# Performance work log

Measured on AMD Instinct MI355X. Metric: run time of the kernel, lower is better.

Reference implementation:

```python
import jax, jax.numpy as jnp
from jax import lax
import numpy as np


def crf_log_likelihood(logits, tags, seqlen, trans):
    # logits [B,T,L], tags [B,T] int, seqlen [B] int, trans [L,L]
    B, T, L = logits.shape
    mask = jnp.arange(T)[None, :] < seqlen[:, None]  # [B,T] bool
    unary = jnp.take_along_axis(logits, tags[..., None], axis=2)[..., 0]  # [B,T]
    unary_score = jnp.sum(unary * mask, axis=1)
    binary = trans[tags[:, :-1], tags[:, 1:]]  # [B,T-1]
    binary_score = jnp.sum(binary * mask[:, 1:], axis=1)

    def step(alpha, inp):
        logit_t, m = inp  # [B,L], [B]
        new = jax.nn.logsumexp(alpha[:, :, None] + trans[None], axis=1) + logit_t
        return jnp.where(m[:, None], new, alpha), None

    xs = (jnp.moveaxis(logits[:, 1:], 1, 0), jnp.moveaxis(mask[:, 1:], 1, 0))
    alphaT, _ = lax.scan(step, logits[:, 0], xs)
    log_norm = jax.nn.logsumexp(alphaT, axis=1)  # [B]
    return unary_score + binary_score - log_norm


def crf_decode(logits, trans, seqlen):
    B, T, L = logits.shape
    mask = jnp.arange(T)[None, :] < seqlen[:, None]
    ident = jnp.broadcast_to(jnp.arange(L)[None, :], (B, L))

    def fwd(alpha, inp):
        logit_t, m = inp
        scores = alpha[:, :, None] + trans[None]  # [B,L,L]
        bp = jnp.argmax(scores, axis=1)  # [B,L] best prev tag for each cur tag
        new = jnp.max(scores, axis=1) + logit_t
        alpha = jnp.where(m[:, None], new, alpha)
        bp = jnp.where(m[:, None], bp, ident)  # identity bp on padded steps
        return alpha, bp

    xs = (jnp.moveaxis(logits[:, 1:], 1, 0), jnp.moveaxis(mask[:, 1:], 1, 0))
    alphaT, bps = lax.scan(fwd, logits[:, 0], xs)  # bps [T-1,B,L]
    last = jnp.argmax(alphaT, axis=1)  # [B]

    def back(tag, bp):
        prev = jnp.take_along_axis(bp, tag[:, None], axis=1)[:, 0]
        return prev, prev

    _, tags_prev = lax.scan(back, last, bps, reverse=True)  # [T-1,B]
    return jnp.concatenate([jnp.moveaxis(tags_prev, 1, 0), last[:, None]], axis=1)


def setup_inputs():
    key = jax.random.key(0)
    ks = jax.random.split(key, 8)
    B, T, D = 64, 512, 768
    L1, L2 = 2, 9
    x = jax.random.normal(ks[0], (B, T, D), dtype=jnp.float32)
    label = jax.random.randint(ks[1], (B, T), 0, L2)
    seqlen = jax.random.randint(ks[2], (B,), 1, T + 1)
    W1 = jax.random.truncated_normal(ks[3], -2.0, 2.0, (D, L1), jnp.float32) * 0.02
    b1 = jnp.zeros((L1,), jnp.float32)
    W2 = jax.random.truncated_normal(ks[4], -2.0, 2.0, (D, L2), jnp.float32) * 0.02
    b2 = jnp.zeros((L2,), jnp.float32)
    lim1 = float(np.sqrt(6.0 / (L1 + L1)))
    trans1 = jax.random.uniform(ks[5], (L1, L1), jnp.float32, -lim1, lim1)
    lim2 = float(np.sqrt(6.0 / (L2 + L2)))
    trans2 = jax.random.uniform(ks[6], (L2, L2), jnp.float32, -lim2, lim2)
    return {"x": x, "label": label, "seqlen": seqlen, "W1": W1, "b1": b1,
            "W2": W2, "b2": b2, "trans1": trans1, "trans2": trans2}


def reference(x, label, seqlen, W1, b1, W2, b2, trans1, trans2):
    T = x.shape[1]
    mask = (jnp.arange(T)[None, :] < seqlen[:, None]).astype(jnp.float32)
    total = jnp.sum(seqlen.astype(jnp.float32))

    label1 = jnp.where(label > 0, jnp.ones_like(label), jnp.zeros_like(label))
    out1 = x @ W1 + b1  # [B,T,2]
    ll1 = crf_log_likelihood(out1, label1, seqlen, trans1)
    loss1 = jnp.mean(-ll1)
    vit1 = crf_decode(out1, trans1, seqlen)
    acc1 = jnp.sum((vit1 == label1).astype(jnp.float32) * mask) / total

    out2 = x @ W2 + b2  # [B,T,9]
    ll2 = crf_log_likelihood(out2, label, seqlen, trans2)
    loss2 = jnp.mean(-ll2)
    vit2 = crf_decode(out2, trans2, seqlen)
    acc2 = jnp.sum((vit2 == label).astype(jnp.float32) * mask) / total

    loss = (loss1 + 8.0 * loss2) / 9.0
    viterbi = jnp.where(vit1 == 0, jnp.zeros_like(vit1), vit2)
    acc = jnp.sum((viterbi == label).astype(jnp.float32) * mask) / total
    return viterbi, loss, acc1, acc2, acc
```

## Files before the change

kernel.cpp:

```cpp
#include <hip/hip_runtime.h>

#define TT 512
#define BB 64
#define DD 768
#define NEG (-1e30f)

__device__ __forceinline__ float fmax3(float a, float b, float c) {
    return fmaxf(fmaxf(a, b), c);
}
__device__ __forceinline__ int imin3(int a, int b, int c) {
    return min(min(a, b), c);
}
__device__ __forceinline__ float rl(float x, int i) {
    return __int_as_float(__builtin_amdgcn_readlane(__float_as_int(x), i));
}
__device__ __forceinline__ float dot4(float4 a, float4 b) {
    return a.x * b.x + a.y * b.y + a.z * b.z + a.w * b.w;
}
__device__ __forceinline__ void gl_lds16(const float* g, float* l) {
    __builtin_amdgcn_global_load_lds(
        (const __attribute__((address_space(1))) void*)g,
        (__attribute__((address_space(3))) void*)l, 16, 0, 0);
}

__global__ __launch_bounds__(256) void gemm_kernel(
    const float* __restrict__ x,
    const float* __restrict__ W1, const float* __restrict__ b1,
    const float* __restrict__ W2, const float* __restrict__ b2,
    float* __restrict__ o1, float* __restrict__ o2)
{
    __shared__ float wT[11][DD];
    __shared__ float x_tile[2][64 * 64];

    const int tid = threadIdx.x;
    const int wave = tid >> 6, lane = tid & 63;

    for (int i = tid; i < 11 * DD; i += 256) {
        int m = i / DD, d = i - m * DD;
        wT[m][d] = (m < 2) ? W1[d * 2 + m] : W2[d * 9 + (m - 2)];
    }

    const int row0 = blockIdx.x * 64;
#define STAGE_TILE(KT, BF) { \
        _Pragma("unroll") \
        for (int i = 0; i < 4; ++i) { \
            const int e = i * 256 + tid; \
            const int r = e >> 4, q = e & 15; \
            const int qg = q ^ (r & 15); \
            const float* gp = x + ((size_t)(row0 + r) * DD + (KT) * 64 + qg * 4); \
            gl_lds16(gp, &x_tile[BF][e * 4]); \
        } }

    STAGE_TILE(0, 0);
    __syncthreads();

    const int c = lane & 7, g = lane >> 3;
    const int rw = wave * 16;

    float acc[2][11];
#pragma unroll
    for (int j = 0; j < 2; ++j)
#pragma unroll
        for (int m = 0; m < 11; ++m) acc[j][m] = 0.f;

    for (int kt = 0; kt < 12; ++kt) {
        const int cur = kt & 1;
        if (kt + 1 < 12) STAGE_TILE(kt + 1, cur ^ 1);

        float4 xa[2], xb[2];
#pragma unroll
        for (int j = 0; j < 2; ++j) {
            const int r = rw + g + 8 * j;
            const int s = r & 15;
            const int pA = (2 * c) ^ s, pB = (2 * c + 1) ^ s;
            xa[j] = *(const float4*)&x_tile[cur][r * 64 + pA * 4];
            xb[j] = *(const float4*)&x_tile[cur][r * 64 + pB * 4];
        }
#pragma unroll
        for (int m = 0; m < 11; ++m) {
            const float* wp = &wT[m][kt * 64 + c * 8];
            float4 wa = *(const float4*)(wp);
            float4 wb = *(const float4*)(wp + 4);
#pragma unroll
            for (int j = 0; j < 2; ++j)
                acc[j][m] += dot4(xa[j], wa) + dot4(xb[j], wb);
        }
        __syncthreads();
    }

#pragma unroll
    for (int j = 0; j < 2; ++j)
#pragma unroll
        for (int m = 0; m < 11; ++m) {
            acc[j][m] += __shfl_xor(acc[j][m], 1);
            acc[j][m] += __shfl_xor(acc[j][m], 2);
            acc[j][m] += __shfl_xor(acc[j][m], 4);
        }

    if (c == 0) {
        float bb1[2] = { b1[0], b1[1] };
        float bb2[9];
#pragma unroll
        for (int m = 0; m < 9; ++m) bb2[m] = b2[m];
#pragma unroll
        for (int j = 0; j < 2; ++j) {
            const int row = row0 + rw + g + 8 * j;
            o1[row * 2 + 0] = acc[j][0] + bb1[0];
            o1[row * 2 + 1] = acc[j][1] + bb1[1];
#pragma unroll
            for (int m = 0; m < 9; ++m) o2[row * 9 + m] = acc[j][m + 2] + bb2[m];
        }
    }
#undef STAGE_TILE
}

__global__ __launch_bounds__(256) void crf_kernel(
    const float* __restrict__ o1, const float* __restrict__ o2,
    const int* __restrict__ label, const int* __restrict__ seqlen,
    const float* __restrict__ trans1, const float* __restrict__ trans2,
    float* __restrict__ dout,
    float* __restrict__ M1, float* __restrict__ M2,
    float* __restrict__ scores, float* __restrict__ counts)
{
    __shared__ float s_l2[TT][9];
    __shared__ float s_l1[TT][2];
    __shared__ float s_alpha2[TT][9];
    __shared__ float s_alpha1[TT][2];
    __shared__ int   s_lab[TT];
    __shared__ float s_tr2[81];
    __shared__ float s_tr1[4];
    __shared__ unsigned char s_bp2[9][TT];
    __shared__ unsigned char s_bp1[2][TT];
    __shared__ unsigned char s_path2[16][9][36];
    __shared__ unsigned char s_path1[16][2][36];
    __shared__ unsigned char s_sel2[16], s_sel1[16];
    __shared__ float s_part[2][4];
    __shared__ int s_last2, s_last1;
    __shared__ int s_cnt[4][3];

    const int tid  = threadIdx.x;
    const int wave = tid >> 6, lane = tid & 63;

    if (blockIdx.x >= 64) {
        const int bc  = blockIdx.x - 64;
        const int b   = bc >> 4, cch = bc & 15;
        const int sl  = seqlen[b];
        const int t0  = cch * 32 + 1;
        const int cap = (cch < 15) ? 32 : 31;
        int n = sl - t0; n = n < 0 ? 0 : (n > cap ? cap : n);

        for (int i = tid; i < cap * 9; i += 256) {
            int t = i / 9, k = i - t * 9;
            s_l2[t][k] = o2[((size_t)b * TT + t0 + t) * 9 + k];
        }
        for (int i = tid; i < cap * 2; i += 256) {
            int t = i >> 1, k = i & 1;
            s_l1[t][k] = o1[((size_t)b * TT + t0 + t) * 2 + k];
        }
        if (tid < 81) s_tr2[tid] = trans2[tid];
        if (tid >= 128 && tid < 132) s_tr1[tid - 128] = trans1[tid - 128];
        __syncthreads();

        if (wave < 2) {
            int L, i_row, jj, base2; bool active;
            if (wave == 0) {
                if (lane < 63) { active = true;  L = 9; i_row = lane / 9; jj = lane - i_row * 9; base2 = i_row * 9; }
                else           { active = false; L = 9; i_row = 0; jj = 0; base2 = 54; }
            } else {
                if (lane < 18)      { active = true;  L = 9; i_row = 7 + lane / 9; jj = lane % 9; base2 = (lane / 9) * 9; }
                else if (lane < 22) { active = true;  L = 2; i_row = (lane - 18) >> 1; jj = (lane - 18) & 1; base2 = 18 + ((lane - 18) & ~1); }
                else                { active = false; L = 2; i_row = 0; jj = 0; base2 = 18; }
            }

            float tcol[9], row[9];
#pragma unroll
            for (int k = 0; k < 9; ++k) {
                tcol[k] = (k < L) ? ((L == 9) ? s_tr2[k * 9 + jj] : s_tr1[k * 2 + jj]) : NEG;
                row[k]  = (k < L && k == i_row) ? 0.f : NEG;
            }
            const float* lp = (L == 9) ? &s_l2[0][jj] : &s_l1[0][jj];
            const int lstride = L;

            for (int tt = 0; tt < n; ++tt) {
                float l = lp[tt * lstride];
                float v[9];
#pragma unroll
                for (int k = 0; k < 9; ++k) v[k] = row[k] + tcol[k];
                float m = fmax3(fmax3(v[0], v[1], v[2]), fmax3(v[3], v[4], v[5]), fmax3(v[6], v[7], v[8]));
                float s = 0.f;
#pragma unroll
                for (int k = 0; k < 9; ++k) s += __expf(v[k] - m);
                float nv = m + __logf(s) + l;
#pragma unroll
                for (int k = 0; k < 9; ++k) {
                    float sv = __shfl(nv, base2 + (k < L ? k : 0));
                    row[k] = (k < L) ? sv : NEG;
                }
            }
            if (active) {
                if (L == 9) M2[((size_t)(b * 16 + cch)) * 81 + i_row * 9 + jj] = row[jj];
                else        M1[((size_t)(b * 16 + cch)) * 4  + i_row * 2 + jj] = row[jj];
            }
        }
        return;
    }

    const int b  = blockIdx.x;
    const int sl = seqlen[b];

    {
        const float4* src = (const float4*)(o2 + (size_t)b * TT * 9);
        float4* dst = (float4*)&s_l2[0][0];
        for (int i = tid; i < TT * 9 / 4; i += 256) dst[i] = src[i];
    }
    {
        const float4* src = (const float4*)(o1 + (size_t)b * TT * 2);
        float4* dst = (float4*)&s_l1[0][0];
        for (int i = tid; i < TT * 2 / 4; i += 256) dst[i] = src[i];
    }
    {
        const int4* src = (const int4*)(label + (size_t)b * TT);
        int4* dst = (int4*)s_lab;
        for (int i = tid; i < TT / 4; i += 256) dst[i] = src[i];
    }
    if (tid < 81) s_tr2[tid] = trans2[tid];
    if (tid >= 96 && tid < 100) s_tr1[tid - 96] = trans1[tid - 96];
    for (int i = tid; i < 9 * TT; i += 256) ((unsigned char*)s_bp2)[i] = (unsigned char)(i >> 9);
    for (int i = tid; i < 2 * TT; i += 256) ((unsigned char*)s_bp1)[i] = (unsigned char)(i >> 9);
    __syncthreads();

    if (wave == 0) {
        if (lane < 9) {
            const int j = lane;
            float tc0 = s_tr2[0 * 9 + j], tc1 = s_tr2[1 * 9 + j], tc2 = s_tr2[2 * 9 + j];
            float tc3 = s_tr2[3 * 9 + j], tc4 = s_tr2[4 * 9 + j], tc5 = s_tr2[5 * 9 + j];
            float tc6 = s_tr2[6 * 9 + j], tc7 = s_tr2[7 * 9 + j], tc8 = s_tr2[8 * 9 + j];
            float av = s_l2[0][j];
            s_alpha2[0][j] = av;
            float a0 = rl(av, 0), a1 = rl(av, 1), a2 = rl(av, 2);
            float a3 = rl(av, 3), a4 = rl(av, 4), a5 = rl(av, 5);
            float a6 = rl(av, 6), a7 = rl(av, 7), a8 = rl(av, 8);

#define VSTEP2(T, LG) { \
            float v0=a0+tc0, v1=a1+tc1, v2=a2+tc2, v3=a3+tc3, v4=a4+tc4; \
            float v5=a5+tc5, v6=a6+tc6, v7=a7+tc7, v8=a8+tc8; \
            float mm = fmax3(fmax3(v0,v1,v2), fmax3(v3,v4,v5), fmax3(v6,v7,v8)); \
            float nj = mm + (LG); \
            s_alpha2[T][j] = nj; \
            a0=rl(nj,0); a1=rl(nj,1); a2=rl(nj,2); a3=rl(nj,3); a4=rl(nj,4); \
            a5=rl(nj,5); a6=rl(nj,6); a7=rl(nj,7); a8=rl(nj,8); }

            for (int t = 1; t < 8 && t < sl; ++t) {
                float lg = s_l2[t][j];
                VSTEP2(t, lg);
            }
            int t0 = 8;
            for (; t0 + 8 <= sl; t0 += 8) {
                float l0 = s_l2[t0 + 0][j], l1 = s_l2[t0 + 1][j];
                float l2 = s_l2[t0 + 2][j], l3 = s_l2[t0 + 3][j];
                float l4 = s_l2[t0 + 4][j], l5 = s_l2[t0 + 5][j];
                float l6 = s_l2[t0 + 6][j], l7 = s_l2[t0 + 7][j];
                VSTEP2(t0 + 0, l0); VSTEP2(t0 + 1, l1);
                VSTEP2(t0 + 2, l2); VSTEP2(t0 + 3, l3);
                VSTEP2(t0 + 4, l4); VSTEP2(t0 + 5, l5);
                VSTEP2(t0 + 6, l6); VSTEP2(t0 + 7, l7);
            }
            for (int t = t0; t < sl; ++t) {
                float lg = s_l2[t][j];
                VSTEP2(t, lg);
            }
#undef VSTEP2
            if (lane == 0) {
                float mm = fmax3(fmax3(a0, a1, a2), fmax3(a3, a4, a5), fmax3(a6, a7, a8));
                int c0 = (a0 == mm) ? 0 : 15, c1 = (a1 == mm) ? 1 : 15, c2 = (a2 == mm) ? 2 : 15;
                int c3 = (a3 == mm) ? 3 : 15, c4 = (a4 == mm) ? 4 : 15, c5 = (a5 == mm) ? 5 : 15;
                int c6 = (a6 == mm) ? 6 : 15, c7 = (a7 == mm) ? 7 : 15, c8 = (a8 == mm) ? 8 : 15;
                s_last2 = imin3(imin3(c0, c1, c2), imin3(c3, c4, c5), imin3(c6, c7, c8));
            }
        }
    } else if (wave == 1) {
        if (lane < 2) {
            const int j = lane;
            float tc0 = s_tr1[0 * 2 + j], tc1 = s_tr1[1 * 2 + j];
            float av = s_l1[0][j];
            s_alpha1[0][j] = av;
            float a0 = rl(av, 0), a1 = rl(av, 1);

#define VSTEP1(T, LG) { \
            float v0 = a0 + tc0, v1 = a1 + tc1; \
            float nj = fmaxf(v0, v1) + (LG); \
            s_alpha1[T][j] = nj; \
            a0 = rl(nj, 0); a1 = rl(nj, 1); }

            for (int t = 1; t < 8 && t < sl; ++t) {
                float lg = s_l1[t][j];
                VSTEP1(t, lg);
            }
            int t0 = 8;
            for (; t0 + 8 <= sl; t0 += 8) {
                float l0 = s_l1[t0 + 0][j], l1 = s_l1[t0 + 1][j];
                float l2 = s_l1[t0 + 2][j], l3 = s_l1[t0 + 3][j];
                float l4 = s_l1[t0 + 4][j], l5 = s_l1[t0 + 5][j];
                float l6 = s_l1[t0 + 6][j], l7 = s_l1[t0 + 7][j];
                VSTEP1(t0 + 0, l0); VSTEP1(t0 + 1, l1);
                VSTEP1(t0 + 2, l2); VSTEP1(t0 + 3, l3);
                VSTEP1(t0 + 4, l4); VSTEP1(t0 + 5, l5);
                VSTEP1(t0 + 6, l6); VSTEP1(t0 + 7, l7);
            }
            for (int t = t0; t < sl; ++t) {
                float lg = s_l1[t][j];
                VSTEP1(t, lg);
            }
#undef VSTEP1
            if (lane == 0) s_last1 = (a1 > a0) ? 1 : 0;
        }
    } else {
        const int t0i = tid - 128;
        float u1 = 0.f, bs1 = 0.f, u2 = 0.f, bs2 = 0.f;
        for (int t = t0i; t < sl; t += 128) {
            int lb = s_lab[t]; int lb1 = lb > 0 ? 1 : 0;
            u1 += s_l1[t][lb1];
            u2 += s_l2[t][lb];
            if (t >= 1) {
                int lp = s_lab[t - 1]; int lp1 = lp > 0 ? 1 : 0;
                bs1 += s_tr1[lp1 * 2 + lb1];
                bs2 += s_tr2[lp * 9 + lb];
            }
        }
        for (int off = 32; off; off >>= 1) {
            u1 += __shfl_down(u1, off); bs1 += __shfl_down(bs1, off);
            u2 += __shfl_down(u2, off); bs2 += __shfl_down(bs2, off);
        }
        if (lane == 0) {
            s_part[wave - 2][0] = u1; s_part[wave - 2][1] = bs1;
            s_part[wave - 2][2] = u2; s_part[wave - 2][3] = bs2;
        }
    }
    __syncthreads();

    if (tid < 252) {
        const int j = tid % 9;
        const int tq = tid / 9;
        float tc0 = s_tr2[0 * 9 + j], tc1 = s_tr2[1 * 9 + j], tc2 = s_tr2[2 * 9 + j];
        float tc3 = s_tr2[3 * 9 + j], tc4 = s_tr2[4 * 9 + j], tc5 = s_tr2[5 * 9 + j];
        float tc6 = s_tr2[6 * 9 + j], tc7 = s_tr2[7 * 9 + j], tc8 = s_tr2[8 * 9 + j];
        for (int t = 1 + tq; t < sl; t += 28) {
            const float* ap = &s_alpha2[t - 1][0];
            float v0 = ap[0] + tc0, v1 = ap[1] + tc1, v2 = ap[2] + tc2;
            float v3 = ap[3] + tc3, v4 = ap[4] + tc4, v5 = ap[5] + tc5;
            float v6 = ap[6] + tc6, v7 = ap[7] + tc7, v8 = ap[8] + tc8;
            float mm = fmax3(fmax3(v0, v1, v2), fmax3(v3, v4, v5), fmax3(v6, v7, v8));
            int c0 = (v0 == mm) ? 0 : 15, c1 = (v1 == mm) ? 1 : 15, c2 = (v2 == mm) ? 2 : 15;
            int c3 = (v3 == mm) ? 3 : 15, c4 = (v4 == mm) ? 4 : 15, c5 = (v5 == mm) ? 5 : 15;
            int c6 = (v6 == mm) ? 6 : 15, c7 = (v7 == mm) ? 7 : 15, c8 = (v8 == mm) ? 8 : 15;
            int bi = imin3(imin3(c0, c1, c2), imin3(c3, c4, c5), imin3(c6, c7, c8));
            s_bp2[j][t] = (unsigned char)bi;
        }
    }
    {
        const int j1 = tid & 1;
        float t10 = s_tr1[0 * 2 + j1], t11 = s_tr1[1 * 2 + j1];
        for (int t = 1 + (tid >> 1); t < sl; t += 128) {
            float v0 = s_alpha1[t - 1][0] + t10;
            float v1 = s_alpha1[t - 1][1] + t11;
            s_bp1[j1][t] = (unsigned char)((v1 > v0) ? 1 : 0);
        }
    }
    __syncthreads();

    if (tid < 144) {
        int cch = tid / 9, e = tid - cch * 9;
        int pe = (cch < 15) ? (cch + 1) * 32 : 511;
        int tag = e;
        for (int t = pe; t > cch * 32; --t) {
            tag = s_bp2[tag][t];
            s_path2[cch][e][t - 1 - cch * 32] = (unsigned char)tag;
        }
    } else if (tid >= 160 && tid < 192) {
        int k = tid - 160, cch = k >> 1, e = k & 1;
        int pe = (cch < 15) ? (cch + 1) * 32 : 511;
        int tag = e;
        for (int t = pe; t > cch * 32; --t) {
            tag = s_bp1[tag][t];
            s_path1[cch][e][t - 1 - cch * 32] = (unsigned char)tag;
        }
    } else if (tid >= 224 && tid < 228) {
        int k = tid - 224;
        scores[b * 4 + k] = s_part[0][k] + s_part[1][k];
    }
    __syncthreads();

    if (tid == 0) {
        int cur = s_last2;
        for (int c = 15; c >= 0; --c) { s_sel2[c] = (unsigned char)cur; cur = s_path2[c][cur][0]; }
    } else if (tid == 1) {
        int cur = s_last1;
        for (int c = 15; c >= 0; --c) { s_sel1[c] = (unsigned char)cur; cur = s_path1[c][cur][0]; }
    }
    __syncthreads();

    {
        int c1 = 0, c2 = 0, cc = 0;
        for (int p = tid; p < TT; p += 256) {
            int ch = p >> 5;
            int v2 = (p == 511) ? s_last2 : (int)s_path2[ch][s_sel2[ch]][p & 31];
            int v1 = (p == 511) ? s_last1 : (int)s_path1[ch][s_sel1[ch]][p & 31];
            int comb = (v1 == 0) ? 0 : v2;
            dout[(size_t)b * TT + p] = (float)comb;
            if (p < sl) {
                int lb = s_lab[p]; int lb1 = lb > 0 ? 1 : 0;
                c1 += (v1 == lb1); c2 += (v2 == lb); cc += (comb == lb);
            }
        }
        for (int off = 32; off; off >>= 1) {
            c1 += __shfl_down(c1, off); c2 += __shfl_down(c2, off); cc += __shfl_down(cc, off);
        }
        if (lane == 0) { s_cnt[wave][0] = c1; s_cnt[wave][1] = c2; s_cnt[wave][2] = cc; }
    }
    __syncthreads();
    if (tid == 0) {
        counts[b * 3 + 0] = (float)(s_cnt[0][0] + s_cnt[1][0] + s_cnt[2][0] + s_cnt[3][0]);
        counts[b * 3 + 1] = (float)(s_cnt[0][1] + s_cnt[1][1] + s_cnt[2][1] + s_cnt[3][1]);
        counts[b * 3 + 2] = (float)(s_cnt[0][2] + s_cnt[1][2] + s_cnt[2][2] + s_cnt[3][2]);
    }
}

__global__ __launch_bounds__(64) void finalize_kernel(
    const float* __restrict__ o1, const float* __restrict__ o2,
    const float* __restrict__ M1, const float* __restrict__ M2,
    const float* __restrict__ scores,
    float* __restrict__ ll1, float* __restrict__ ll2)
{
    __shared__ float sM2[16 * 81];
    __shared__ float sM1[16 * 4];
    const int s = blockIdx.x, lane = threadIdx.x;

    for (int i = lane; i < 16 * 81; i += 64) sM2[i] = M2[(size_t)s * 16 * 81 + i];
    for (int i = lane; i < 16 * 4;  i += 64) sM1[i] = M1[(size_t)s * 16 * 4 + i];
    __syncthreads();

    if (lane < 9) {
        const int r = lane;
        float av = o2[(size_t)s * TT * 9 + r];
        float a0 = rl(av, 0), a1 = rl(av, 1), a2 = rl(av, 2);
        float a3 = rl(av, 3), a4 = rl(av, 4), a5 = rl(av, 5);
        float a6 = rl(av, 6), a7 = rl(av, 7), a8 = rl(av, 8);
        for (int c = 0; c < 16; ++c) {
            const float* M = &sM2[c * 81];
            float v0 = a0 + M[0 * 9 + r], v1 = a1 + M[1 * 9 + r], v2 = a2 + M[2 * 9 + r];
            float v3 = a3 + M[3 * 9 + r], v4 = a4 + M[4 * 9 + r], v5 = a5 + M[5 * 9 + r];
            float v6 = a6 + M[6 * 9 + r], v7 = a7 + M[7 * 9 + r], v8 = a8 + M[8 * 9 + r];
            float m = fmax3(fmax3(v0, v1, v2), fmax3(v3, v4, v5), fmax3(v6, v7, v8));
            float su = __expf(v0 - m) + __expf(v1 - m) + __expf(v2 - m)
                     + __expf(v3 - m) + __expf(v4 - m) + __expf(v5 - m)
                     + __expf(v6 - m) + __expf(v7 - m) + __expf(v8 - m);
            float na = m + __logf(su);
            a0 = rl(na, 0); a1 = rl(na, 1); a2 = rl(na, 2);
            a3 = rl(na, 3); a4 = rl(na, 4); a5 = rl(na, 5);
            a6 = rl(na, 6); a7 = rl(na, 7); a8 = rl(na, 8);
        }
        if (lane == 0) {
            float m = fmax3(fmax3(a0, a1, a2), fmax3(a3, a4, a5), fmax3(a6, a7, a8));
            float su = __expf(a0 - m) + __expf(a1 - m) + __expf(a2 - m)
                     + __expf(a3 - m) + __expf(a4 - m) + __expf(a5 - m)
                     + __expf(a6 - m) + __expf(a7 - m) + __expf(a8 - m);
            float ln = m + __logf(su);
            ll2[s] = (scores[s * 4 + 2] + scores[s * 4 + 3]) - ln;
        }
    } else if (lane >= 16 && lane < 18) {
        const int jj = lane - 16;
        float av = o1[(size_t)s * TT * 2 + jj];
        float a0 = rl(av, 16), a1 = rl(av, 17);
        for (int c = 0; c < 16; ++c) {
            const float* M = &sM1[c * 4];
            float v0 = a0 + M[0 * 2 + jj], v1 = a1 + M[1 * 2 + jj];
            float mm = fmaxf(v0, v1);
            float na = mm + __logf(__expf(v0 - mm) + __expf(v1 - mm));
            a0 = rl(na, 16); a1 = rl(na, 17);
        }
        if (jj == 0) {
            float mm = fmaxf(a0, a1);
            float ln = mm + __logf(__expf(a0 - mm) + __expf(a1 - mm));
            ll1[s] = (scores[s * 4 + 0] + scores[s * 4 + 1]) - ln;
        }
    }
}

__global__ __launch_bounds__(64) void reduce_kernel(
    const float* __restrict__ ll1, const float* __restrict__ ll2,
    const float* __restrict__ counts, const int* __restrict__ seqlen,
    float* __restrict__ out)
{
    const int t = threadIdx.x;
    float v1 = ll1[t], v2 = ll2[t];
    float a1 = counts[t * 3 + 0], a2 = counts[t * 3 + 1], ac = counts[t * 3 + 2];
    float slf = (float)seqlen[t];
    for (int off = 32; off; off >>= 1) {
        v1 += __shfl_down(v1, off); v2 += __shfl_down(v2, off);
        a1 += __shfl_down(a1, off); a2 += __shfl_down(a2, off);
        ac += __shfl_down(ac, off); slf += __shfl_down(slf, off);
    }
    if (t == 0) {
        float loss1 = -v1 / 64.f;
        float loss2 = -v2 / 64.f;
        out[BB * TT + 0] = (loss1 + 8.f * loss2) / 9.f;
        out[BB * TT + 1] = a1 / slf;
        out[BB * TT + 2] = a2 / slf;
        out[BB * TT + 3] = ac / slf;
    }
}

extern "C" void kernel_launch(void* const* d_in, const int* in_sizes, int n_in,
                              void* d_out, int out_size, void* d_ws, size_t ws_size,
                              hipStream_t stream) {
    (void)in_sizes; (void)n_in; (void)out_size; (void)ws_size;
    const float* x      = (const float*)d_in[0];
    const int*   label  = (const int*)d_in[1];
    const int*   seqlen = (const int*)d_in[2];
    const float* W1     = (const float*)d_in[3];
    const float* b1     = (const float*)d_in[4];
    const float* W2     = (const float*)d_in[5];
    const float* b2     = (const float*)d_in[6];
    const float* trans1 = (const float*)d_in[7];
    const float* trans2 = (const float*)d_in[8];
    float* out = (float*)d_out;
    float* ws  = (float*)d_ws;

    float* o1     = ws;
    float* o2     = o1 + BB * TT * 2;
    float* M2     = o2 + BB * TT * 9;
    float* M1     = M2 + 64 * 16 * 81;
    float* scores = M1 + 64 * 16 * 4;
    float* counts = scores + 64 * 4;
    float* ll1    = counts + 64 * 3;
    float* ll2    = ll1 + BB;

    gemm_kernel<<<512, 256, 0, stream>>>(x, W1, b1, W2, b2, o1, o2);
    crf_kernel<<<1088, 256, 0, stream>>>(o1, o2, label, seqlen, trans1, trans2,
                                         out, M1, M2, scores, counts);
    finalize_kernel<<<64, 64, 0, stream>>>(o1, o2, M1, M2, scores, ll1, ll2);
    reduce_kernel<<<1, 64, 0, stream>>>(ll1, ll2, counts, seqlen, out);
}
```

Baseline: 220.1 us.

## Fuse chunked logsumexp transfer matrices into GEMM epilogue and merge finalize into Viterbi

The per-chunk forward-algorithm transfer matrices move into the epilogue of the GEMM kernel. Each GEMM block covers 64 timesteps of one sequence, so two teams of two waves each compute 32-step chunks straight from shared memory. The separate finalize kernel is removed and its chunk-combine logsumexp now runs inside the Viterbi kernel on otherwise idle threads. Backpointer workers are rebalanced to make room for it. This saves one launch and a global round trip, but the serial chunk scan now sits in the GEMM tail, which may lengthen that kernel.

New measurement: 228.9 us. 1.04x slower.

```diff
diff --git a/kernel.cpp b/kernel.cpp
--- a/kernel.cpp
+++ b/kernel.cpp
@@ -23,14 +23,19 @@
         (__attribute__((address_space(3))) void*)l, 16, 0, 0);
 }
 
-__global__ __launch_bounds__(256) void gemm_kernel(
+__global__ __launch_bounds__(256) void gemm_lse_kernel(
     const float* __restrict__ x,
     const float* __restrict__ W1, const float* __restrict__ b1,
     const float* __restrict__ W2, const float* __restrict__ b2,
-    float* __restrict__ o1, float* __restrict__ o2)
+    const int* __restrict__ seqlen,
+    const float* __restrict__ trans1, const float* __restrict__ trans2,
+    float* __restrict__ o1, float* __restrict__ o2,
+    float* __restrict__ M1, float* __restrict__ M2)
 {
     __shared__ float wT[11][DD];
     __shared__ float x_tile[2][64 * 64];
+    __shared__ float s_l2[64][9];
+    __shared__ float s_l1[64][2];
 
     const int tid = threadIdx.x;
     const int wave = tid >> 6, lane = tid & 63;
@@ -104,23 +109,78 @@
         for (int m = 0; m < 9; ++m) bb2[m] = b2[m];
 #pragma unroll
         for (int j = 0; j < 2; ++j) {
-            const int row = row0 + rw + g + 8 * j;
-            o1[row * 2 + 0] = acc[j][0] + bb1[0];
-            o1[row * 2 + 1] = acc[j][1] + bb1[1];
-#pragma unroll
-            for (int m = 0; m < 9; ++m) o2[row * 9 + m] = acc[j][m + 2] + bb2[m];
-        }
+            const int tl = rw + g + 8 * j;
+            const int row = row0 + tl;
+            float v0 = acc[j][0] + bb1[0], v1 = acc[j][1] + bb1[1];
+            o1[row * 2 + 0] = v0; o1[row * 2 + 1] = v1;
+            s_l1[tl][0] = v0;     s_l1[tl][1] = v1;
+#pragma unroll
+            for (int m = 0; m < 9; ++m) {
+                float vv = acc[j][m + 2] + bb2[m];
+                o2[row * 9 + m] = vv;
+                s_l2[tl][m] = vv;
+            }
+        }
+    }
+    __syncthreads();
+
+    const int b = blockIdx.x >> 3, k = blockIdx.x & 7;
+    const int sl = seqlen[b];
+    const int team = wave >> 1;
+    const int wpar = wave & 1;
+    const int cch = 2 * k + team;
+    const int t0c = cch * 32;
+    int tstart = (t0c < 1) ? 1 : t0c;
+    int tend = t0c + 32; if (tend > sl) tend = sl;
+
+    int L, i_row, jj, base2; bool active;
+    if (wpar == 0) {
+        if (lane < 63) { active = true;  L = 9; i_row = lane / 9; jj = lane - i_row * 9; base2 = i_row * 9; }
+        else           { active = false; L = 9; i_row = 0; jj = 0; base2 = 54; }
+    } else {
+        if (lane < 18)      { active = true;  L = 9; i_row = 7 + lane / 9; jj = lane % 9; base2 = (lane / 9) * 9; }
+        else if (lane < 22) { active = true;  L = 2; i_row = (lane - 18) >> 1; jj = (lane - 18) & 1; base2 = 18 + ((lane - 18) & ~1); }
+        else                { active = false; L = 2; i_row = 0; jj = 0; base2 = 18; }
+    }
+
+    float tcol[9], row[9];
+#pragma unroll
+    for (int q = 0; q < 9; ++q) {
+        tcol[q] = (q < L) ? ((L == 9) ? trans2[q * 9 + jj] : trans1[q * 2 + jj]) : NEG;
+        row[q]  = (q < L && q == i_row) ? 0.f : NEG;
+    }
+
+    for (int t = tstart; t < tend; ++t) {
+        const int tl = t - k * 64;
+        float l = (L == 9) ? s_l2[tl][jj] : s_l1[tl][jj];
+        float v[9];
+#pragma unroll
+        for (int q = 0; q < 9; ++q) v[q] = row[q] + tcol[q];
+        float m = fmax3(fmax3(v[0], v[1], v[2]), fmax3(v[3], v[4], v[5]), fmax3(v[6], v[7], v[8]));
+        float s = 0.f;
+#pragma unroll
+        for (int q = 0; q < 9; ++q) s += __expf(v[q] - m);
+        float nv = m + __logf(s) + l;
+#pragma unroll
+        for (int q = 0; q < 9; ++q) {
+            float sv = __shfl(nv, base2 + (q < L ? q : 0));
+            row[q] = (q < L) ? sv : NEG;
+        }
+    }
+    if (active) {
+        if (L == 9) M2[((size_t)(b * 16 + cch)) * 81 + i_row * 9 + jj] = row[jj];
+        else        M1[((size_t)(b * 16 + cch)) * 4  + i_row * 2 + jj] = row[jj];
     }
 #undef STAGE_TILE
 }
 
-__global__ __launch_bounds__(256) void crf_kernel(
+__global__ __launch_bounds__(256) void viterbi_kernel(
     const float* __restrict__ o1, const float* __restrict__ o2,
     const int* __restrict__ label, const int* __restrict__ seqlen,
     const float* __restrict__ trans1, const float* __restrict__ trans2,
+    const float* __restrict__ M1, const float* __restrict__ M2,
     float* __restrict__ dout,
-    float* __restrict__ M1, float* __restrict__ M2,
-    float* __restrict__ scores, float* __restrict__ counts)
+    float* __restrict__ counts, float* __restrict__ ll1, float* __restrict__ ll2)
 {
     __shared__ float s_l2[TT][9];
     __shared__ float s_l1[TT][2];
@@ -129,6 +189,8 @@
     __shared__ int   s_lab[TT];
     __shared__ float s_tr2[81];
     __shared__ float s_tr1[4];
+    __shared__ float sM2[16 * 81];
+    __shared__ float sM1[16 * 4];
     __shared__ unsigned char s_bp2[9][TT];
     __shared__ unsigned char s_bp1[2][TT];
     __shared__ unsigned char s_path2[16][9][36];
@@ -140,71 +202,6 @@
 
     const int tid  = threadIdx.x;
     const int wave = tid >> 6, lane = tid & 63;
-
-    if (blockIdx.x >= 64) {
-        const int bc  = blockIdx.x - 64;
-        const int b   = bc >> 4, cch = bc & 15;
-        const int sl  = seqlen[b];
-        const int t0  = cch * 32 + 1;
-        const int cap = (cch < 15) ? 32 : 31;
-        int n = sl - t0; n = n < 0 ? 0 : (n > cap ? cap : n);
-
-        for (int i = tid; i < cap * 9; i += 256) {
-            int t = i / 9, k = i - t * 9;
-            s_l2[t][k] = o2[((size_t)b * TT + t0 + t) * 9 + k];
-        }
-        for (int i = tid; i < cap * 2; i += 256) {
-            int t = i >> 1, k = i & 1;
-            s_l1[t][k] = o1[((size_t)b * TT + t0 + t) * 2 + k];
-        }
-        if (tid < 81) s_tr2[tid] = trans2[tid];
-        if (tid >= 128 && tid < 132) s_tr1[tid - 128] = trans1[tid - 128];
-        __syncthreads();
-
-        if (wave < 2) {
-            int L, i_row, jj, base2; bool active;
-            if (wave == 0) {
-                if (lane < 63) { active = true;  L = 9; i_row = lane / 9; jj = lane - i_row * 9; base2 = i_row * 9; }
-                else           { active = false; L = 9; i_row = 0; jj = 0; base2 = 54; }
-            } else {
-                if (lane < 18)      { active = true;  L = 9; i_row = 7 + lane / 9; jj = lane % 9; base2 = (lane / 9) * 9; }
-                else if (lane < 22) { active = true;  L = 2; i_row = (lane - 18) >> 1; jj = (lane - 18) & 1; base2 = 18 + ((lane - 18) & ~1); }
-                else                { active = false; L = 2; i_row = 0; jj = 0; base2 = 18; }
-            }
-
-            float tcol[9], row[9];
-#pragma unroll
-            for (int k = 0; k < 9; ++k) {
-                tcol[k] = (k < L) ? ((L == 9) ? s_tr2[k * 9 + jj] : s_tr1[k * 2 + jj]) : NEG;
-                row[k]  = (k < L && k == i_row) ? 0.f : NEG;
-            }
-            const float* lp = (L == 9) ? &s_l2[0][jj] : &s_l1[0][jj];
-            const int lstride = L;
-
-            for (int tt = 0; tt < n; ++tt) {
-                float l = lp[tt * lstride];
-                float v[9];
-#pragma unroll
-                for (int k = 0; k < 9; ++k) v[k] = row[k] + tcol[k];
-                float m = fmax3(fmax3(v[0], v[1], v[2]), fmax3(v[3], v[4], v[5]), fmax3(v[6], v[7], v[8]));
-                float s = 0.f;
-#pragma unroll
-                for (int k = 0; k < 9; ++k) s += __expf(v[k] - m);
-                float nv = m + __logf(s) + l;
-#pragma unroll
-                for (int k = 0; k < 9; ++k) {
-                    float sv = __shfl(nv, base2 + (k < L ? k : 0));
-                    row[k] = (k < L) ? sv : NEG;
-                }
-            }
-            if (active) {
-                if (L == 9) M2[((size_t)(b * 16 + cch)) * 81 + i_row * 9 + jj] = row[jj];
-                else        M1[((size_t)(b * 16 + cch)) * 4  + i_row * 2 + jj] = row[jj];
-            }
-        }
-        return;
-    }
-
     const int b  = blockIdx.x;
     const int sl = seqlen[b];
 
@@ -223,6 +220,8 @@
         int4* dst = (int4*)s_lab;
         for (int i = tid; i < TT / 4; i += 256) dst[i] = src[i];
     }
+    for (int i = tid; i < 16 * 81; i += 256) sM2[i] = M2[(size_t)b * 16 * 81 + i];
+    for (int i = tid; i < 16 * 4;  i += 256) sM1[i] = M1[(size_t)b * 16 * 4 + i];
     if (tid < 81) s_tr2[tid] = trans2[tid];
     if (tid >= 96 && tid < 100) s_tr1[tid - 96] = trans1[tid - 96];
     for (int i = tid; i < 9 * TT; i += 256) ((unsigned char*)s_bp2)[i] = (unsigned char)(i >> 9);
@@ -338,13 +337,13 @@
     }
     __syncthreads();
 
-    if (tid < 252) {
+    if (tid < 189) {
         const int j = tid % 9;
         const int tq = tid / 9;
         float tc0 = s_tr2[0 * 9 + j], tc1 = s_tr2[1 * 9 + j], tc2 = s_tr2[2 * 9 + j];
         float tc3 = s_tr2[3 * 9 + j], tc4 = s_tr2[4 * 9 + j], tc5 = s_tr2[5 * 9 + j];
         float tc6 = s_tr2[6 * 9 + j], tc7 = s_tr2[7 * 9 + j], tc8 = s_tr2[8 * 9 + j];
-        for (int t = 1 + tq; t < sl; t += 28) {
+        for (int t = 1 + tq; t < sl; t += 21) {
             const float* ap = &s_alpha2[t - 1][0];
             float v0 = ap[0] + tc0, v1 = ap[1] + tc1, v2 = ap[2] + tc2;
             float v3 = ap[3] + tc3, v4 = ap[4] + tc4, v5 = ap[5] + tc5;
@@ -356,14 +355,58 @@
             int bi = imin3(imin3(c0, c1, c2), imin3(c3, c4, c5), imin3(c6, c7, c8));
             s_bp2[j][t] = (unsigned char)bi;
         }
-    }
-    {
-        const int j1 = tid & 1;
+    } else if (tid >= 192 && tid < 224) {
+        const int kk = tid - 192;
+        const int j1 = kk & 1, tq = kk >> 1;
         float t10 = s_tr1[0 * 2 + j1], t11 = s_tr1[1 * 2 + j1];
-        for (int t = 1 + (tid >> 1); t < sl; t += 128) {
+        for (int t = 1 + tq; t < sl; t += 16) {
             float v0 = s_alpha1[t - 1][0] + t10;
             float v1 = s_alpha1[t - 1][1] + t11;
             s_bp1[j1][t] = (unsigned char)((v1 > v0) ? 1 : 0);
+        }
+    } else if (tid >= 224 && tid < 233) {
+        const int r = tid - 224;
+        float av = s_l2[0][r];
+        float a0 = rl(av, 32), a1 = rl(av, 33), a2 = rl(av, 34);
+        float a3 = rl(av, 35), a4 = rl(av, 36), a5 = rl(av, 37);
+        float a6 = rl(av, 38), a7 = rl(av, 39), a8 = rl(av, 40);
+        for (int cc = 0; cc < 16; ++cc) {
+            const float* M = &sM2[cc * 81];
+            float v0 = a0 + M[0 * 9 + r], v1 = a1 + M[1 * 9 + r], v2 = a2 + M[2 * 9 + r];
+            float v3 = a3 + M[3 * 9 + r], v4 = a4 + M[4 * 9 + r], v5 = a5 + M[5 * 9 + r];
+            float v6 = a6 + M[6 * 9 + r], v7 = a7 + M[7 * 9 + r], v8 = a8 + M[8 * 9 + r];
+            float m = fmax3(fmax3(v0, v1, v2), fmax3(v3, v4, v5), fmax3(v6, v7, v8));
+            float su = __expf(v0 - m) + __expf(v1 - m) + __expf(v2 - m)
+                     + __expf(v3 - m) + __expf(v4 - m) + __expf(v5 - m)
+                     + __expf(v6 - m) + __expf(v7 - m) + __expf(v8 - m);
+            float na = m + __logf(su);
+            a0 = rl(na, 32); a1 = rl(na, 33); a2 = rl(na, 34);
+            a3 = rl(na, 35); a4 = rl(na, 36); a5 = rl(na, 37);
+            a6 = rl(na, 38); a7 = rl(na, 39); a8 = rl(na, 40);
+        }
+        if (r == 0) {
+            float m = fmax3(fmax3(a0, a1, a2), fmax3(a3, a4, a5), fmax3(a6, a7, a8));
+            float su = __expf(a0 - m) + __expf(a1 - m) + __expf(a2 - m)
+                     + __expf(a3 - m) + __expf(a4 - m) + __expf(a5 - m)
+                     + __expf(a6 - m) + __expf(a7 - m) + __expf(a8 - m);
+            float ln = m + __logf(su);
+            ll2[b] = (s_part[0][2] + s_part[1][2] + s_part[0][3] + s_part[1][3]) - ln;
+        }
+    } else if (tid >= 240 && tid < 242) {
+        const int jj = tid - 240;
+        float av = s_l1[0][jj];
+        float a0 = rl(av, 48), a1 = rl(av, 49);
+        for (int cc = 0; cc < 16; ++cc) {
+            const float* M = &sM1[cc * 4];
+            float v0 = a0 + M[0 * 2 + jj], v1 = a1 + M[1 * 2 + jj];
+            float mm = fmaxf(v0, v1);
+            float na = mm + __logf(__expf(v0 - mm) + __expf(v1 - mm));
+            a0 = rl(na, 48); a1 = rl(na, 49);
+        }
+        if (jj == 0) {
+            float mm = fmaxf(a0, a1);
+            float ln = mm + __logf(__expf(a0 - mm) + __expf(a1 - mm));
+            ll1[b] = (s_part[0][0] + s_part[1][0] + s_part[0][1] + s_part[1][1]) - ln;
         }
     }
     __syncthreads();
@@ -384,9 +427,6 @@
             tag = s_bp1[tag][t];
             s_path1[cch][e][t - 1 - cch * 32] = (unsigned char)tag;
         }
-    } else if (tid >= 224 && tid < 228) {
-        int k = tid - 224;
-        scores[b * 4 + k] = s_part[0][k] + s_part[1][k];
     }
     __syncthreads();
 
@@ -422,67 +462,6 @@
         counts[b * 3 + 0] = (float)(s_cnt[0][0] + s_cnt[1][0] + s_cnt[2][0] + s_cnt[3][0]);
         counts[b * 3 + 1] = (float)(s_cnt[0][1] + s_cnt[1][1] + s_cnt[2][1] + s_cnt[3][1]);
         counts[b * 3 + 2] = (float)(s_cnt[0][2] + s_cnt[1][2] + s_cnt[2][2] + s_cnt[3][2]);
-    }
-}
-
-__global__ __launch_bounds__(64) void finalize_kernel(
-    const float* __restrict__ o1, const float* __restrict__ o2,
-    const float* __restrict__ M1, const float* __restrict__ M2,
-    const float* __restrict__ scores,
-    float* __restrict__ ll1, float* __restrict__ ll2)
-{
-    __shared__ float sM2[16 * 81];
-    __shared__ float sM1[16 * 4];
-    const int s = blockIdx.x, lane = threadIdx.x;
-
-    for (int i = lane; i < 16 * 81; i += 64) sM2[i] = M2[(size_t)s * 16 * 81 + i];
-    for (int i = lane; i < 16 * 4;  i += 64) sM1[i] = M1[(size_t)s * 16 * 4 + i];
-    __syncthreads();
-
-    if (lane < 9) {
-        const int r = lane;
-        float av = o2[(size_t)s * TT * 9 + r];
-        float a0 = rl(av, 0), a1 = rl(av, 1), a2 = rl(av, 2);
-        float a3 = rl(av, 3), a4 = rl(av, 4), a5 = rl(av, 5);
-        float a6 = rl(av, 6), a7 = rl(av, 7), a8 = rl(av, 8);
-        for (int c = 0; c < 16; ++c) {
-            const float* M = &sM2[c * 81];
-            float v0 = a0 + M[0 * 9 + r], v1 = a1 + M[1 * 9 + r], v2 = a2 + M[2 * 9 + r];
-            float v3 = a3 + M[3 * 9 + r], v4 = a4 + M[4 * 9 + r], v5 = a5 + M[5 * 9 + r];
-            float v6 = a6 + M[6 * 9 + r], v7 = a7 + M[7 * 9 + r], v8 = a8 + M[8 * 9 + r];
-            float m = fmax3(fmax3(v0, v1, v2), fmax3(v3, v4, v5), fmax3(v6, v7, v8));
-            float su = __expf(v0 - m) + __expf(v1 - m) + __expf(v2 - m)
-                     + __expf(v3 - m) + __expf(v4 - m) + __expf(v5 - m)
-                     + __expf(v6 - m) + __expf(v7 - m) + __expf(v8 - m);
-            float na = m + __logf(su);
-            a0 = rl(na, 0); a1 = rl(na, 1); a2 = rl(na, 2);
-            a3 = rl(na, 3); a4 = rl(na, 4); a5 = rl(na, 5);
-            a6 = rl(na, 6); a7 = rl(na, 7); a8 = rl(na, 8);
-        }
-        if (lane == 0) {
-            float m = fmax3(fmax3(a0, a1, a2), fmax3(a3, a4, a5), fmax3(a6, a7, a8));
-            float su = __expf(a0 - m) + __expf(a1 - m) + __expf(a2 - m)
-                     + __expf(a3 - m) + __expf(a4 - m) + __expf(a5 - m)
-                     + __expf(a6 - m) + __expf(a7 - m) + __expf(a8 - m);
-            float ln = m + __logf(su);
-            ll2[s] = (scores[s * 4 + 2] + scores[s * 4 + 3]) - ln;
-        }
-    } else if (lane >= 16 && lane < 18) {
-        const int jj = lane - 16;
-        float av = o1[(size_t)s * TT * 2 + jj];
-        float a0 = rl(av, 16), a1 = rl(av, 17);
-        for (int c = 0; c < 16; ++c) {
-            const float* M = &sM1[c * 4];
-            float v0 = a0 + M[0 * 2 + jj], v1 = a1 + M[1 * 2 + jj];
-            float mm = fmaxf(v0, v1);
-            float na = mm + __logf(__expf(v0 - mm) + __expf(v1 - mm));
-            a0 = rl(na, 16); a1 = rl(na, 17);
-        }
-        if (jj == 0) {
-            float mm = fmaxf(a0, a1);
-            float ln = mm + __logf(__expf(a0 - mm) + __expf(a1 - mm));
-            ll1[s] = (scores[s * 4 + 0] + scores[s * 4 + 1]) - ln;
-        }
     }
 }
 
@@ -530,14 +509,13 @@
     float* o2     = o1 + BB * TT * 2;
     float* M2     = o2 + BB * TT * 9;
     float* M1     = M2 + 64 * 16 * 81;
-    float* scores = M1 + 64 * 16 * 4;
-    float* counts = scores + 64 * 4;
+    float* counts = M1 + 64 * 16 * 4;
     float* ll1    = counts + 64 * 3;
     float* ll2    = ll1 + BB;
 
-    gemm_kernel<<<512, 256, 0, stream>>>(x, W1, b1, W2, b2, o1, o2);
-    crf_kernel<<<1088, 256, 0, stream>>>(o1, o2, label, seqlen, trans1, trans2,
-                                         out, M1, M2, scores, counts);
-    finalize_kernel<<<64, 64, 0, stream>>>(o1, o2, M1, M2, scores, ll1, ll2);
+    gemm_lse_kernel<<<512, 256, 0, stream>>>(x, W1, b1, W2, b2, seqlen,
+                                             trans1, trans2, o1, o2, M1, M2);
+    viterbi_kernel<<<64, 256, 0, stream>>>(o1, o2, label, seqlen, trans1, trans2,
+                                           M1, M2, out, counts, ll1, ll2);
     reduce_kernel<<<1, 64, 0, stream>>>(ll1, ll2, counts, seqlen, out);
 }
```
